# Kernel optimization log

Hardware: AMD Instinct MI355X
Metric: run time of the kernel (lower is better)

The kernel has to match this reference:

```python
import jax, jax.numpy as jnp
import numpy as np

HEADS = 12
HEAD_SIZE = 64
NEG_BIG = 1e12


def _rope_sincos(n, head_size, dtype):
    # rotary position embeddings: (n, head_size) each, with each freq repeated twice
    pos = jnp.arange(n, dtype=dtype)
    inv = jnp.power(10000.0, -2.0 * jnp.arange(head_size // 2, dtype=dtype) / head_size)
    emb = pos[:, None] * inv[None, :]               # (n, head_size//2)
    sin = jnp.repeat(jnp.sin(emb), 2, axis=-1)       # (n, head_size)
    cos = jnp.repeat(jnp.cos(emb), 2, axis=-1)
    return sin, cos


def _rotate_half(x):
    # stack([-x[...,1::2], x[...,::2]], -1).reshape_as(x)
    x2 = jnp.stack([-x[..., 1::2], x[..., ::2]], axis=-1)
    return x2.reshape(x.shape)


def setup_inputs() -> dict:
    key = jax.random.key(0)
    k1, k2, k3 = jax.random.split(key, 3)
    b, n, h = 16, 512, 1024
    inputs = jax.random.normal(k1, (b, n, h), dtype=jnp.float32)
    attention_mask = jnp.ones((b, n), dtype=jnp.float32)
    W1 = jax.random.normal(k2, (h, 2 * HEAD_SIZE), dtype=jnp.float32) * (1.0 / np.sqrt(h))
    b1 = jnp.zeros((2 * HEAD_SIZE,), dtype=jnp.float32)
    W2 = jax.random.normal(k3, (2 * HEAD_SIZE, 2 * HEADS), dtype=jnp.float32) * (1.0 / np.sqrt(2 * HEAD_SIZE))
    b2 = jnp.zeros((2 * HEADS,), dtype=jnp.float32)
    return {"inputs": inputs, "attention_mask": attention_mask,
            "W1": W1, "b1": b1, "W2": W2, "b2": b2}


def reference(inputs, attention_mask, W1, b1, W2, b2):
    b, n, _ = inputs.shape
    x = inputs @ W1 + b1                              # (b, n, 2*head_size)
    qw, kw = x[..., ::2], x[..., 1::2]                # (b, n, head_size)

    sin, cos = _rope_sincos(n, HEAD_SIZE, x.dtype)    # (n, head_size)
    qw = qw * cos[None] + _rotate_half(qw) * sin[None]
    kw = kw * cos[None] + _rotate_half(kw) * sin[None]

    logits = jnp.einsum('bmd,bnd->bmn', qw, kw) / (HEAD_SIZE ** 0.5)  # (b, n, n)

    bias = (x @ W2 + b2).transpose(0, 2, 1) / 2.0     # (b, 2*heads, n)
    logits = logits[:, None] + bias[:, ::2, None, :] + bias[:, 1::2, :, None]  # (b, heads, n, n)

    attn = 1.0 - attention_mask[:, None, None, :] * attention_mask[:, None, :, None]
    logits = logits - attn * NEG_BIG

    tril = jnp.tril(jnp.ones((n, n), dtype=logits.dtype), k=-1)
    logits = logits - tril[None, None] * NEG_BIG
    return logits
```

## Files before the change

### kernel.cpp

```cpp
#include <hip/hip_runtime.h>
#include <math.h>

#define NB 16
#define SEQ 512
#define HID 1024
#define XDIM 128
#define NHEADS 12
#define NROWS (NB*SEQ)
#define NEG_BIG 1000000000000.0f
#define MTILE 16

typedef __bf16 bf16x8 __attribute__((ext_vector_type(8)));
typedef __bf16 bf16x4 __attribute__((ext_vector_type(4)));
typedef float  f32x4  __attribute__((ext_vector_type(4)));

__global__ __launch_bounds__(256) void egp_prep(
    const float* __restrict__ W1, __bf16* __restrict__ W1T)
{
    int idx = blockIdx.x * 256 + threadIdx.x;
    int n   = idx >> 7;
    int k0  = (idx & 127) << 3;
    bf16x8 o;
    #pragma unroll
    for (int j = 0; j < 8; j++)
        o[j] = (__bf16)W1[(size_t)(k0 + j) * XDIM + n];
    *(bf16x8*)(W1T + (size_t)n * HID + k0) = o;
}

__global__ __launch_bounds__(256) void egp_stage1(
    const float* __restrict__ inp,
    const __bf16* __restrict__ W1T,
    const float* __restrict__ b1,
    const float* __restrict__ W2,
    const float* __restrict__ b2,
    __bf16* __restrict__ qw,
    __bf16* __restrict__ kw,
    float* __restrict__ biasw)
{
    __shared__ __bf16 As[2048];
    __shared__ float  Xs[MTILE][132];
    __shared__ float  W2s[XDIM * 24];
    __shared__ float  b2s[24];

    const int t    = threadIdx.x;
    const int row0 = blockIdx.x * MTILE;
    const int lane = t & 63;
    const int w    = t >> 6;
    const int quad = lane >> 4;
    const int mrow = lane & 15;
    const int ncol0 = w * 32;

    for (int i = t; i < XDIM * 24; i += 256) W2s[i] = W2[i];
    if (t < 24) b2s[t] = b2[t];

    const int m_st = t >> 4;
    const int k_st = (t & 15) * 4;
    const int s_st  = k_st >> 5;
    const int q_st  = (k_st & 31) >> 3;
    const int j_st  = k_st & 7;
    const int off_st = s_st * 1024 + q_st * 128 + m_st * 8 + j_st;
    const float* aptr = inp + (size_t)(row0 + m_st) * HID + k_st;

    float4 v[16];
    #pragma unroll
    for (int c = 0; c < 16; c++)
        v[c] = *(const float4*)(aptr + 64 * c);

    f32x4 acc0 = {0.f, 0.f, 0.f, 0.f};
    f32x4 acc1 = {0.f, 0.f, 0.f, 0.f};

    #pragma unroll
    for (int c = 0; c < 16; c++) {
        const int kc = c * 64;
        __syncthreads();
        bf16x4 p;
        p[0] = (__bf16)v[c].x; p[1] = (__bf16)v[c].y;
        p[2] = (__bf16)v[c].z; p[3] = (__bf16)v[c].w;
        *(bf16x4*)(&As[off_st]) = p;
        __syncthreads();

        #pragma unroll
        for (int s2 = 0; s2 < 2; s2++) {
            bf16x8 a = *(bf16x8*)(&As[s2 * 1024 + quad * 128 + mrow * 8]);
            {
                const __bf16* bp = W1T + (size_t)(ncol0 + mrow) * HID
                                 + kc + s2 * 32 + quad * 8;
                bf16x8 b = *(const bf16x8*)(bp);
                acc0 = __builtin_amdgcn_mfma_f32_16x16x32_bf16(a, b, acc0, 0, 0, 0);
            }
            {
                const __bf16* bp = W1T + (size_t)(ncol0 + 16 + mrow) * HID
                                 + kc + s2 * 32 + quad * 8;
                bf16x8 b = *(const bf16x8*)(bp);
                acc1 = __builtin_amdgcn_mfma_f32_16x16x32_bf16(a, b, acc1, 0, 0, 0);
            }
        }
    }

    float b1v0 = b1[ncol0 + mrow];
    float b1v1 = b1[ncol0 + 16 + mrow];
    #pragma unroll
    for (int r = 0; r < 4; r++) {
        Xs[quad * 4 + r][ncol0 + mrow]      = acc0[r] + b1v0;
        Xs[quad * 4 + r][ncol0 + 16 + mrow] = acc1[r] + b1v1;
    }
    __syncthreads();

    const int tx = t & 15;
    const int r  = t >> 4;
    const float LOG1E4 = 9.210340371976184f;
    float inv0 = expf(-((float)(2 * tx)     * (1.0f / 32.0f)) * LOG1E4);
    float inv1 = expf(-((float)(2 * tx + 1) * (1.0f / 32.0f)) * LOG1E4);
    {
        int grow  = row0 + r;
        float pos = (float)(grow & (SEQ - 1));
        float x[8];
        #pragma unroll
        for (int j = 0; j < 8; j++) x[j] = Xs[r][tx * 8 + j];
        float s0 = sinf(pos * inv0), c0 = cosf(pos * inv0);
        float s1 = sinf(pos * inv1), c1 = cosf(pos * inv1);
        bf16x4 q4, k4;
        q4[0] = (__bf16)(x[0] * c0 - x[2] * s0);
        q4[1] = (__bf16)(x[2] * c0 + x[0] * s0);
        q4[2] = (__bf16)(x[4] * c1 - x[6] * s1);
        q4[3] = (__bf16)(x[6] * c1 + x[4] * s1);
        k4[0] = (__bf16)(x[1] * c0 - x[3] * s0);
        k4[1] = (__bf16)(x[3] * c0 + x[1] * s0);
        k4[2] = (__bf16)(x[5] * c1 - x[7] * s1);
        k4[3] = (__bf16)(x[7] * c1 + x[5] * s1);
        *(bf16x4*)(qw + (size_t)grow * 64 + tx * 4) = q4;
        *(bf16x4*)(kw + (size_t)grow * 64 + tx * 4) = k4;
    }

    for (int o = t; o < MTILE * 24; o += 256) {
        int row = o / 24;
        int jj  = o - row * 24;
        float s = 0.0f;
        for (int kk = 0; kk < XDIM; kk++)
            s += Xs[row][kk] * W2s[kk * 24 + jj];
        biasw[(size_t)(row0 + row) * 24 + jj] = (s + b2s[jj]) * 0.5f;
    }
}

__global__ __launch_bounds__(256) void egp_stage2(
    const __bf16* __restrict__ qw,
    const __bf16* __restrict__ kw,
    const float* __restrict__ biasw,
    const float* __restrict__ am,
    float* __restrict__ out)
{
    __shared__ float Vals[MTILE][516];
    __shared__ float bEs[NHEADS][512];
    __shared__ float bOs[NHEADS][MTILE];
    __shared__ float amN[512];
    __shared__ float amM[MTILE];

    const int b  = blockIdx.y;
    const int m0 = blockIdx.x * MTILE;
    const int t  = threadIdx.x;
    const int lane = t & 63;
    const int w    = t >> 6;
    const int quad = lane >> 4;
    const int l16  = lane & 15;

    #pragma unroll
    for (int u = 0; u < 2; u++) amN[t + 256 * u] = am[b * SEQ + t + 256 * u];
    if (t < MTILE) amM[t] = am[b * SEQ + m0 + t];
    for (int o = t; o < NHEADS * MTILE; o += 256) {
        int h  = o >> 4;
        int mm = o & 15;
        bOs[h][mm] = biasw[(size_t)(b * SEQ + m0 + mm) * 24 + 2 * h + 1];
    }
    for (int o = t; o < NHEADS * 512; o += 256) {
        int h = o >> 9;
        int n = o & 511;
        bEs[h][n] = biasw[(size_t)(b * SEQ + n) * 24 + 2 * h];
    }

    const __bf16* qbase = qw + ((size_t)(b * SEQ + m0 + l16)) * 64 + quad * 8;
    bf16x8 a0 = *(const bf16x8*)(qbase);
    bf16x8 a1 = *(const bf16x8*)(qbase + 32);

    f32x4 acc[8];
    #pragma unroll
    for (int u = 0; u < 8; u++) {
        int nt = w * 8 + u;
        const __bf16* kbase = kw + ((size_t)(b * SEQ + nt * 16 + l16)) * 64 + quad * 8;
        bf16x8 b0 = *(const bf16x8*)(kbase);
        bf16x8 b1 = *(const bf16x8*)(kbase + 32);
        f32x4 z = {0.f, 0.f, 0.f, 0.f};
        z = __builtin_amdgcn_mfma_f32_16x16x32_bf16(a0, b0, z, 0, 0, 0);
        z = __builtin_amdgcn_mfma_f32_16x16x32_bf16(a1, b1, z, 0, 0, 0);
        acc[u] = z;
    }

    #pragma unroll
    for (int u = 0; u < 8; u++) {
        int n = w * 128 + u * 16 + l16;
        float an = amN[n];
        #pragma unroll
        for (int r = 0; r < 4; r++) {
            int mloc = quad * 4 + r;
            int m    = m0 + mloc;
            float msk = (1.0f - amM[mloc] * an) * NEG_BIG
                      + ((n < m) ? NEG_BIG : 0.0f);
            Vals[mloc][n] = acc[u][r] * 0.125f - msk;
        }
    }
    __syncthreads();

    #pragma unroll
    for (int h = 0; h < NHEADS; h++) {
        float* hbase = out + ((size_t)((b * NHEADS + h) * SEQ + m0)) * SEQ;
        #pragma unroll
        for (int it = 0; it < 8; it++) {
            int f4   = t + 256 * it;
            int row  = f4 >> 7;
            int col4 = f4 & 127;
            float4 v = *(const float4*)(&Vals[row][col4 * 4]);
            float4 e = *(const float4*)(&bEs[h][col4 * 4]);
            float  bo = bOs[h][row];
            float4 o4;
            o4.x = v.x + e.x + bo;
            o4.y = v.y + e.y + bo;
            o4.z = v.z + e.z + bo;
            o4.w = v.w + e.w + bo;
            *(float4*)(hbase + (size_t)f4 * 4) = o4;
        }
    }
}

extern "C" void kernel_launch(void* const* d_in, const int* in_sizes, int n_in,
                              void* d_out, int out_size, void* d_ws, size_t ws_size,
                              hipStream_t stream) {
    const float* inp = (const float*)d_in[0];
    const float* am  = (const float*)d_in[1];
    const float* W1  = (const float*)d_in[2];
    const float* b1  = (const float*)d_in[3];
    const float* W2  = (const float*)d_in[4];
    const float* b2  = (const float*)d_in[5];
    float* out = (float*)d_out;

    __bf16* qw   = (__bf16*)d_ws;
    __bf16* kw   = qw + (size_t)NROWS * 64;
    float*  bias = (float*)(kw + (size_t)NROWS * 64);
    __bf16* w1t  = (__bf16*)(bias + (size_t)NROWS * 24);

    egp_prep<<<64, 256, 0, stream>>>(W1, w1t);
    egp_stage1<<<NROWS / MTILE, 256, 0, stream>>>(inp, w1t, b1, W2, b2, qw, kw, bias);

    dim3 g2(SEQ / MTILE, NB);
    egp_stage2<<<g2, 256, 0, stream>>>(qw, kw, bias, am, out);
}
```

Baseline: 263.4 us.

## Stream stage1 A operand from global, transpose bias buffer, nontemporal output stores

```diff
diff --git a/kernel.cpp b/kernel.cpp
--- a/kernel.cpp
+++ b/kernel.cpp
@@ -35,74 +35,51 @@
     const float* __restrict__ b2,
     __bf16* __restrict__ qw,
     __bf16* __restrict__ kw,
-    float* __restrict__ biasw)
+    float* __restrict__ biasT)
 {
-    __shared__ __bf16 As[2048];
-    __shared__ float  Xs[MTILE][132];
-    __shared__ float  W2s[XDIM * 24];
-    __shared__ float  b2s[24];
+    __shared__ float Xs[MTILE][132];
+    __shared__ float W2s[XDIM * 24];
+    __shared__ float b2s[24];
 
     const int t    = threadIdx.x;
     const int row0 = blockIdx.x * MTILE;
     const int lane = t & 63;
     const int w    = t >> 6;
     const int quad = lane >> 4;
-    const int mrow = lane & 15;
+    const int l16  = lane & 15;
     const int ncol0 = w * 32;
 
     for (int i = t; i < XDIM * 24; i += 256) W2s[i] = W2[i];
     if (t < 24) b2s[t] = b2[t];
 
-    const int m_st = t >> 4;
-    const int k_st = (t & 15) * 4;
-    const int s_st  = k_st >> 5;
-    const int q_st  = (k_st & 31) >> 3;
-    const int j_st  = k_st & 7;
-    const int off_st = s_st * 1024 + q_st * 128 + m_st * 8 + j_st;
-    const float* aptr = inp + (size_t)(row0 + m_st) * HID + k_st;
-
-    float4 v[16];
-    #pragma unroll
-    for (int c = 0; c < 16; c++)
-        v[c] = *(const float4*)(aptr + 64 * c);
+    const float*  arow  = inp + (size_t)(row0 + l16) * HID + quad * 8;
+    const __bf16* brow0 = W1T + (size_t)(ncol0 + l16) * HID + quad * 8;
+    const __bf16* brow1 = brow0 + (size_t)16 * HID;
 
     f32x4 acc0 = {0.f, 0.f, 0.f, 0.f};
     f32x4 acc1 = {0.f, 0.f, 0.f, 0.f};
 
-    #pragma unroll
-    for (int c = 0; c < 16; c++) {
-        const int kc = c * 64;
-        __syncthreads();
-        bf16x4 p;
-        p[0] = (__bf16)v[c].x; p[1] = (__bf16)v[c].y;
-        p[2] = (__bf16)v[c].z; p[3] = (__bf16)v[c].w;
-        *(bf16x4*)(&As[off_st]) = p;
-        __syncthreads();
-
-        #pragma unroll
-        for (int s2 = 0; s2 < 2; s2++) {
-            bf16x8 a = *(bf16x8*)(&As[s2 * 1024 + quad * 128 + mrow * 8]);
-            {
-                const __bf16* bp = W1T + (size_t)(ncol0 + mrow) * HID
-                                 + kc + s2 * 32 + quad * 8;
-                bf16x8 b = *(const bf16x8*)(bp);
-                acc0 = __builtin_amdgcn_mfma_f32_16x16x32_bf16(a, b, acc0, 0, 0, 0);
-            }
-            {
-                const __bf16* bp = W1T + (size_t)(ncol0 + 16 + mrow) * HID
-                                 + kc + s2 * 32 + quad * 8;
-                bf16x8 b = *(const bf16x8*)(bp);
-                acc1 = __builtin_amdgcn_mfma_f32_16x16x32_bf16(a, b, acc1, 0, 0, 0);
-            }
-        }
-    }
-
-    float b1v0 = b1[ncol0 + mrow];
-    float b1v1 = b1[ncol0 + 16 + mrow];
+    #pragma unroll 4
+    for (int kc = 0; kc < HID; kc += 32) {
+        float4 af0 = *(const float4*)(arow + kc);
+        float4 af1 = *(const float4*)(arow + kc + 4);
+        bf16x8 a;
+        a[0] = (__bf16)af0.x; a[1] = (__bf16)af0.y;
+        a[2] = (__bf16)af0.z; a[3] = (__bf16)af0.w;
+        a[4] = (__bf16)af1.x; a[5] = (__bf16)af1.y;
+        a[6] = (__bf16)af1.z; a[7] = (__bf16)af1.w;
+        bf16x8 b0 = *(const bf16x8*)(brow0 + kc);
+        bf16x8 b1f = *(const bf16x8*)(brow1 + kc);
+        acc0 = __builtin_amdgcn_mfma_f32_16x16x32_bf16(a, b0,  acc0, 0, 0, 0);
+        acc1 = __builtin_amdgcn_mfma_f32_16x16x32_bf16(a, b1f, acc1, 0, 0, 0);
+    }
+
+    float b1v0 = b1[ncol0 + l16];
+    float b1v1 = b1[ncol0 + 16 + l16];
     #pragma unroll
     for (int r = 0; r < 4; r++) {
-        Xs[quad * 4 + r][ncol0 + mrow]      = acc0[r] + b1v0;
-        Xs[quad * 4 + r][ncol0 + 16 + mrow] = acc1[r] + b1v1;
+        Xs[quad * 4 + r][ncol0 + l16]      = acc0[r] + b1v0;
+        Xs[quad * 4 + r][ncol0 + 16 + l16] = acc1[r] + b1v1;
     }
     __syncthreads();
 
@@ -136,16 +113,17 @@
         int row = o / 24;
         int jj  = o - row * 24;
         float s = 0.0f;
+        #pragma unroll
         for (int kk = 0; kk < XDIM; kk++)
             s += Xs[row][kk] * W2s[kk * 24 + jj];
-        biasw[(size_t)(row0 + row) * 24 + jj] = (s + b2s[jj]) * 0.5f;
+        biasT[(size_t)jj * NROWS + row0 + row] = (s + b2s[jj]) * 0.5f;
     }
 }
 
 __global__ __launch_bounds__(256) void egp_stage2(
     const __bf16* __restrict__ qw,
     const __bf16* __restrict__ kw,
-    const float* __restrict__ biasw,
+    const float* __restrict__ biasT,
     const float* __restrict__ am,
     float* __restrict__ out)
 {
@@ -163,18 +141,19 @@
     const int quad = lane >> 4;
     const int l16  = lane & 15;
 
-    #pragma unroll
-    for (int u = 0; u < 2; u++) amN[t + 256 * u] = am[b * SEQ + t + 256 * u];
+    if (t < 128)
+        *(f32x4*)(&amN[t * 4]) = *(const f32x4*)(am + b * SEQ + t * 4);
     if (t < MTILE) amM[t] = am[b * SEQ + m0 + t];
     for (int o = t; o < NHEADS * MTILE; o += 256) {
         int h  = o >> 4;
         int mm = o & 15;
-        bOs[h][mm] = biasw[(size_t)(b * SEQ + m0 + mm) * 24 + 2 * h + 1];
-    }
-    for (int o = t; o < NHEADS * 512; o += 256) {
-        int h = o >> 9;
-        int n = o & 511;
-        bEs[h][n] = biasw[(size_t)(b * SEQ + n) * 24 + 2 * h];
+        bOs[h][mm] = biasT[(size_t)(2 * h + 1) * NROWS + b * SEQ + m0 + mm];
+    }
+    for (int o = t; o < NHEADS * 128; o += 256) {
+        int h  = o >> 7;
+        int n4 = o & 127;
+        *(f32x4*)(&bEs[h][n4 * 4]) =
+            *(const f32x4*)(biasT + (size_t)(2 * h) * NROWS + b * SEQ + n4 * 4);
     }
 
     const __bf16* qbase = qw + ((size_t)(b * SEQ + m0 + l16)) * 64 + quad * 8;
@@ -187,12 +166,14 @@
         int nt = w * 8 + u;
         const __bf16* kbase = kw + ((size_t)(b * SEQ + nt * 16 + l16)) * 64 + quad * 8;
         bf16x8 b0 = *(const bf16x8*)(kbase);
-        bf16x8 b1 = *(const bf16x8*)(kbase + 32);
+        bf16x8 b1f = *(const bf16x8*)(kbase + 32);
         f32x4 z = {0.f, 0.f, 0.f, 0.f};
-        z = __builtin_amdgcn_mfma_f32_16x16x32_bf16(a0, b0, z, 0, 0, 0);
-        z = __builtin_amdgcn_mfma_f32_16x16x32_bf16(a1, b1, z, 0, 0, 0);
+        z = __builtin_amdgcn_mfma_f32_16x16x32_bf16(a0, b0,  z, 0, 0, 0);
+        z = __builtin_amdgcn_mfma_f32_16x16x32_bf16(a1, b1f, z, 0, 0, 0);
         acc[u] = z;
     }
+
+    __syncthreads();
 
     #pragma unroll
     for (int u = 0; u < 8; u++) {
@@ -209,23 +190,23 @@
     }
     __syncthreads();
 
+    const int col4 = t & 127;
+    const int r0   = t >> 7;
+    f32x4 v[8];
+    #pragma unroll
+    for (int it = 0; it < 8; it++)
+        v[it] = *(const f32x4*)(&Vals[r0 + 2 * it][col4 * 4]);
+
+    float* obase = out + ((size_t)(b * NHEADS) * SEQ + m0) * SEQ + (size_t)t * 4;
     #pragma unroll
     for (int h = 0; h < NHEADS; h++) {
-        float* hbase = out + ((size_t)((b * NHEADS + h) * SEQ + m0)) * SEQ;
+        f32x4 e = *(const f32x4*)(&bEs[h][col4 * 4]);
+        float* hbase = obase + (size_t)h * SEQ * SEQ;
         #pragma unroll
         for (int it = 0; it < 8; it++) {
-            int f4   = t + 256 * it;
-            int row  = f4 >> 7;
-            int col4 = f4 & 127;
-            float4 v = *(const float4*)(&Vals[row][col4 * 4]);
-            float4 e = *(const float4*)(&bEs[h][col4 * 4]);
-            float  bo = bOs[h][row];
-            float4 o4;
-            o4.x = v.x + e.x + bo;
-            o4.y = v.y + e.y + bo;
-            o4.z = v.z + e.z + bo;
-            o4.w = v.w + e.w + bo;
-            *(float4*)(hbase + (size_t)f4 * 4) = o4;
+            float bo = bOs[h][r0 + 2 * it];
+            f32x4 o4 = v[it] + e + bo;
+            __builtin_nontemporal_store(o4, (f32x4*)(hbase + (size_t)it * 1024));
         }
     }
 }
```

Measured after the change: 269.5 us. 2.3% more time.
